# Kernel optimization log

Measured on AMD Instinct MI355X. Metric: run time of the kernel, lower is better.

Reference implementation:

```python
import jax, jax.numpy as jnp
import numpy as np

N = 50000        # num nodes
NFEAT = 512      # input feature dim
NCLASS = 256     # output classes (out_features of out_att)
E_RAND = 800000  # random edges; + N self-loops
NEG_SLOPE = 0.2  # leakyrelu alpha


def setup_inputs() -> dict:
    key = jax.random.key(0)
    k1, k2, k3, k4 = jax.random.split(key, 4)
    x = jax.random.normal(k1, (N, NFEAT), dtype=jnp.float32)
    W = jax.random.normal(k2, (NFEAT, NCLASS), dtype=jnp.float32) / np.float32(np.sqrt(NFEAT))
    a = jax.random.normal(k3, (2 * NCLASS,), dtype=jnp.float32) / np.float32(np.sqrt(2 * NCLASS))
    rand_edges = jax.random.randint(k4, (2, E_RAND), 0, N, dtype=jnp.int32)
    self_loops = jnp.tile(jnp.arange(N, dtype=jnp.int32), (2, 1))
    edge_index = jnp.concatenate([rand_edges, self_loops], axis=1)  # [2, E]
    return {"x": x, "W": W, "a": a, "edge_index": edge_index}


def reference(x, W, a, edge_index):
    # Eval-mode SpGAT: dropout is identity (training=False).
    row, col = edge_index[0], edge_index[1]  # edge = adj.nonzero().t(): row aggregates from col
    h = x @ W                                # [N, F]
    F_out = h.shape[1]
    # a @ cat(h[row], h[col]) == (h @ a1)[row] + (h @ a2)[col]  (avoids [E, 2F] concat)
    s_row = h @ a[:F_out]                    # [N]
    s_col = h @ a[F_out:]                    # [N]
    logits = s_row[row] + s_col[col]         # [E]
    e = jnp.exp(-jax.nn.leaky_relu(logits, negative_slope=NEG_SLOPE))  # [E]
    rowsum = jax.ops.segment_sum(e, row, num_segments=N)               # [N]
    msgs = e[:, None] * h[col]                                         # [E, F]
    h_prime = jax.ops.segment_sum(msgs, row, num_segments=N) / rowsum[:, None]
    return jax.nn.log_softmax(jax.nn.elu(h_prime), axis=1)
```

## Files before the change

### kernel.cpp

```cpp
#include <hip/hip_runtime.h>
#include <math.h>

#define NNODES   50000
#define NFEAT    512
#define NCLASS   256
#define NEG_SLOPE 0.2f
#define GBLK     782
#define SBLK     196
#define BCAP     64

typedef __attribute__((ext_vector_type(8))) short short8;
typedef __attribute__((ext_vector_type(4))) float floatx4;

__device__ __forceinline__ unsigned short f2bf(float f) {
    unsigned u = __builtin_bit_cast(unsigned, f);
    u += 0x7fffu + ((u >> 16) & 1u);
    return (unsigned short)(u >> 16);
}
__device__ __forceinline__ float bf2f_lo(unsigned u) {
    return __builtin_bit_cast(float, u << 16);
}
__device__ __forceinline__ float bf2f_hi(unsigned u) {
    return __builtin_bit_cast(float, u & 0xffff0000u);
}
__device__ __forceinline__ unsigned pack_bf16_rh(float lo, float hi) {
    const unsigned ulo = __builtin_bit_cast(unsigned, lo) + 0x8000u;
    const unsigned uhi = __builtin_bit_cast(unsigned, hi) + 0x8000u;
    return __builtin_amdgcn_perm(uhi, ulo, 0x07060302);
}

#if __has_builtin(__builtin_amdgcn_fdot2_f32_bf16)
#define HAVE_DOT2 1
typedef __attribute__((ext_vector_type(2))) __bf16 bfx2;
__device__ __forceinline__ float dot2bf(unsigned hpair, unsigned epair, float acc) {
    return __builtin_amdgcn_fdot2_f32_bf16(__builtin_bit_cast(bfx2, hpair),
                                           __builtin_bit_cast(bfx2, epair), acc, false);
}
#endif

__global__ __launch_bounds__(256) void init_kernel(const float* __restrict__ W,
                                                   unsigned short* __restrict__ Wt,
                                                   int* __restrict__ cursor, int zn) {
    const int i = blockIdx.x * 256 + threadIdx.x;
    const int n = i >> 9;
    const int k = i & 511;
    Wt[i] = f2bf(W[(size_t)k * NCLASS + n]);
    if (i < zn) cursor[i] = 0;
}

__global__ __launch_bounds__(256, 4) void gemm_scatter_kernel(const float* __restrict__ x,
                                                              const unsigned short* __restrict__ Wt,
                                                              unsigned short* __restrict__ hb,
                                                              const float* __restrict__ a,
                                                              float* __restrict__ s_row,
                                                              float* __restrict__ s_col,
                                                              const int* __restrict__ erow,
                                                              const int* __restrict__ ecol,
                                                              int* __restrict__ cursor,
                                                              int* __restrict__ bucket,
                                                              int M, int E) {
    __shared__ union {
        struct { short As[2][64 * 32]; short Bs[2][256 * 32]; } k;
        short Cs[32 * 260];
    } u;

    const int bid = blockIdx.x;
    const int tid = threadIdx.x;

    if (bid < SBLK) {
        const int stride = SBLK * 256;
        for (int i = bid * 256 + tid; i < E; i += stride) {
            const int r = erow[i];
            const int c = ecol[i];
            const int pos = atomicAdd(&cursor[r], 1);
            if (pos < BCAP) bucket[((size_t)r << 6) + pos] = c;
        }
        return;
    }

    const int w    = tid >> 6;
    const int lane = tid & 63;
    const int rowbase = (bid - SBLK) * 64;

    const int wm = w & 1;
    const int wn = w >> 1;
    const int srow = lane >> 2;
    const int skq  = (lane & 3) << 3;
    const int fm = lane & 15;
    const int fq = lane >> 4;

    floatx4 acc[2][8];
#pragma unroll
    for (int i = 0; i < 2; ++i)
#pragma unroll
        for (int j = 0; j < 8; ++j)
            acc[i][j] = (floatx4){0.f, 0.f, 0.f, 0.f};

    const int arow = min(rowbase + w * 16 + srow, M - 1);
    const size_t abase = (size_t)arow * NFEAT + skq;
    const int lrowA = (w * 16 + srow) * 32 + skq;

#define STAGE_B(buf, k0)                                                                      \
    {                                                                                         \
        _Pragma("unroll")                                                                     \
        for (int t = 0; t < 4; ++t) {                                                         \
            const int seg = w * 4 + t;                                                        \
            const int nr  = seg * 16 + srow;                                                  \
            __builtin_amdgcn_global_load_lds(                                                 \
                (const __attribute__((address_space(1))) void*)(Wt + (size_t)nr * NFEAT + (k0) + skq), \
                (__attribute__((address_space(3))) void*)(&u.k.Bs[buf][seg * 512]), 16, 0, 0); \
        }                                                                                     \
    }

    STAGE_B(0, 0)
    {
        const float4* xp = (const float4*)&x[abase];
        const float4 u0 = xp[0];
        const float4 u1 = xp[1];
        uint4 o;
        o.x = pack_bf16_rh(u0.x, u0.y);
        o.y = pack_bf16_rh(u0.z, u0.w);
        o.z = pack_bf16_rh(u1.x, u1.y);
        o.w = pack_bf16_rh(u1.z, u1.w);
        *(uint4*)&u.k.As[0][lrowA] = o;
    }
    __syncthreads();

    int cur = 0;
    for (int k0 = 0; k0 < NFEAT; k0 += 32) {
        const int nxt = cur ^ 1;
        const bool have_next = (k0 + 32) < NFEAT;
        float4 p0, p1;
        if (have_next) {
            const float4* xp = (const float4*)&x[abase + k0 + 32];
            p0 = xp[0];
            p1 = xp[1];
            STAGE_B(nxt, k0 + 32)
        }

        short8 af[2];
#pragma unroll
        for (int mt = 0; mt < 2; ++mt)
            af[mt] = *(const short8*)&u.k.As[cur][(wm * 32 + mt * 16 + fm) * 32 + fq * 8];
#pragma unroll
        for (int nt = 0; nt < 8; ++nt) {
            const short8 bfr = *(const short8*)&u.k.Bs[cur][(wn * 128 + nt * 16 + fm) * 32 + fq * 8];
            acc[0][nt] = __builtin_amdgcn_mfma_f32_16x16x32_bf16(af[0], bfr, acc[0][nt], 0, 0, 0);
            acc[1][nt] = __builtin_amdgcn_mfma_f32_16x16x32_bf16(af[1], bfr, acc[1][nt], 0, 0, 0);
        }

        if (have_next) {
            uint4 o;
            o.x = pack_bf16_rh(p0.x, p0.y);
            o.y = pack_bf16_rh(p0.z, p0.w);
            o.z = pack_bf16_rh(p1.x, p1.y);
            o.w = pack_bf16_rh(p1.z, p1.w);
            *(uint4*)&u.k.As[nxt][lrowA] = o;
        }
        __syncthreads();
        cur = nxt;
    }

#pragma unroll
    for (int p = 0; p < 2; ++p) {
        __syncthreads();
        if (wm == p) {
#pragma unroll
            for (int mt = 0; mt < 2; ++mt)
#pragma unroll
                for (int nt = 0; nt < 8; ++nt)
#pragma unroll
                    for (int r = 0; r < 4; ++r)
                        u.Cs[(mt * 16 + fq * 4 + r) * 260 + wn * 128 + nt * 16 + fm] =
                            (short)f2bf(acc[mt][nt][r]);
        }
        __syncthreads();
#pragma unroll
        for (int kk = 0; kk < 8; ++kk) {
            const int idx = tid + kk * 256;
            const int lrow = idx >> 6;
            const int c4 = (idx & 63) << 2;
            const int grow = rowbase + p * 32 + lrow;
            const uint2 vv = *(const uint2*)&u.Cs[lrow * 260 + c4];
            const float f0 = bf2f_lo(vv.x), f1 = bf2f_hi(vv.x);
            const float f2 = bf2f_lo(vv.y), f3 = bf2f_hi(vv.y);
            const float4 A1 = *(const float4*)&a[c4];
            const float4 A2 = *(const float4*)&a[NCLASS + c4];
            float p1 = f0 * A1.x + f1 * A1.y + f2 * A1.z + f3 * A1.w;
            float p2 = f0 * A2.x + f1 * A2.y + f2 * A2.z + f3 * A2.w;
#pragma unroll
            for (int off = 1; off < 64; off <<= 1) {
                p1 += __shfl_xor(p1, off);
                p2 += __shfl_xor(p2, off);
            }
            if (grow < M) {
                *(uint2*)&hb[(size_t)grow * NCLASS + c4] = vv;
                if (lane == 0) {
                    s_row[grow] = p1;
                    s_col[grow] = p2;
                }
            }
        }
    }
}

__global__ __launch_bounds__(256) void aggregate_kernel(const unsigned short* __restrict__ hb,
                                                        const int* __restrict__ bucket,
                                                        const int* __restrict__ cnt,
                                                        const float* __restrict__ s_row,
                                                        const float* __restrict__ s_col,
                                                        float* __restrict__ out, int n) {
    const int wave = (int)((blockIdx.x * (size_t)blockDim.x + threadIdx.x) >> 6);
    const int lane = threadIdx.x & 63;
    if (wave >= n) return;
    const int r = wave;
    const int jb = r << 6;
    const int je = jb + min(cnt[r], BCAP);
    const int fo = lane << 2;
    const float sr = s_row[r];

    float rowsum = 0.f;
    int j = jb;

#define EDGE_E(c) ({ const float _l = sr + s_col[c];                         \
                     const float _lr = _l > 0.f ? _l : NEG_SLOPE * _l;       \
                     __expf(-_lr); })

#ifdef HAVE_DOT2
    float ac0 = 0.f, ac1 = 0.f, ac2 = 0.f, ac3 = 0.f;
    for (; j + 3 < je; j += 4) {
        const int4 cv = *(const int4*)&bucket[j];
        const uint2 g0 = *(const uint2*)&hb[(size_t)cv.x * NCLASS + fo];
        const uint2 g1 = *(const uint2*)&hb[(size_t)cv.y * NCLASS + fo];
        const uint2 g2 = *(const uint2*)&hb[(size_t)cv.z * NCLASS + fo];
        const uint2 g3 = *(const uint2*)&hb[(size_t)cv.w * NCLASS + fo];
        const float e0 = EDGE_E(cv.x);
        const float e1 = EDGE_E(cv.y);
        const float e2 = EDGE_E(cv.z);
        const float e3 = EDGE_E(cv.w);
        const unsigned ep01 = pack_bf16_rh(e0, e1);
        const unsigned ep23 = pack_bf16_rh(e2, e3);
        rowsum += (e0 + e1) + (e2 + e3);
        ac0 = dot2bf(__builtin_amdgcn_perm(g1.x, g0.x, 0x05040100), ep01, ac0);
        ac1 = dot2bf(__builtin_amdgcn_perm(g1.x, g0.x, 0x07060302), ep01, ac1);
        ac2 = dot2bf(__builtin_amdgcn_perm(g1.y, g0.y, 0x05040100), ep01, ac2);
        ac3 = dot2bf(__builtin_amdgcn_perm(g1.y, g0.y, 0x07060302), ep01, ac3);
        ac0 = dot2bf(__builtin_amdgcn_perm(g3.x, g2.x, 0x05040100), ep23, ac0);
        ac1 = dot2bf(__builtin_amdgcn_perm(g3.x, g2.x, 0x07060302), ep23, ac1);
        ac2 = dot2bf(__builtin_amdgcn_perm(g3.y, g2.y, 0x05040100), ep23, ac2);
        ac3 = dot2bf(__builtin_amdgcn_perm(g3.y, g2.y, 0x07060302), ep23, ac3);
    }
    float4 acc = make_float4(ac0, ac1, ac2, ac3);
#else
    float4 acc = make_float4(0.f, 0.f, 0.f, 0.f);
    for (; j + 3 < je; j += 4) {
        const int4 cv = *(const int4*)&bucket[j];
        const uint2 g0 = *(const uint2*)&hb[(size_t)cv.x * NCLASS + fo];
        const uint2 g1 = *(const uint2*)&hb[(size_t)cv.y * NCLASS + fo];
        const uint2 g2 = *(const uint2*)&hb[(size_t)cv.z * NCLASS + fo];
        const uint2 g3 = *(const uint2*)&hb[(size_t)cv.w * NCLASS + fo];
        const float e0 = EDGE_E(cv.x);
        const float e1 = EDGE_E(cv.y);
        const float e2 = EDGE_E(cv.z);
        const float e3 = EDGE_E(cv.w);
        rowsum += (e0 + e1) + (e2 + e3);
        acc.x += e0 * bf2f_lo(g0.x) + e1 * bf2f_lo(g1.x) + e2 * bf2f_lo(g2.x) + e3 * bf2f_lo(g3.x);
        acc.y += e0 * bf2f_hi(g0.x) + e1 * bf2f_hi(g1.x) + e2 * bf2f_hi(g2.x) + e3 * bf2f_hi(g3.x);
        acc.z += e0 * bf2f_lo(g0.y) + e1 * bf2f_lo(g1.y) + e2 * bf2f_lo(g2.y) + e3 * bf2f_lo(g3.y);
        acc.w += e0 * bf2f_hi(g0.y) + e1 * bf2f_hi(g1.y) + e2 * bf2f_hi(g2.y) + e3 * bf2f_hi(g3.y);
    }
#endif
    for (; j < je; ++j) {
        const int c = bucket[j];
        const uint2 g = *(const uint2*)&hb[(size_t)c * NCLASS + fo];
        const float e = EDGE_E(c);
        rowsum += e;
        acc.x += e * bf2f_lo(g.x);
        acc.y += e * bf2f_hi(g.x);
        acc.z += e * bf2f_lo(g.y);
        acc.w += e * bf2f_hi(g.y);
    }

    const float inv = 1.f / rowsum;
    float v[4] = {acc.x * inv, acc.y * inv, acc.z * inv, acc.w * inv};
#pragma unroll
    for (int i = 0; i < 4; ++i)
        v[i] = v[i] > 0.f ? v[i] : __expf(v[i]) - 1.f;

    float m = fmaxf(fmaxf(v[0], v[1]), fmaxf(v[2], v[3]));
#pragma unroll
    for (int off = 32; off > 0; off >>= 1) m = fmaxf(m, __shfl_xor(m, off));
    float s = 0.f;
#pragma unroll
    for (int i = 0; i < 4; ++i) s += __expf(v[i] - m);
#pragma unroll
    for (int off = 32; off > 0; off >>= 1) s += __shfl_xor(s, off);
    const float lse = m + __logf(s);

    float4 o = make_float4(v[0] - lse, v[1] - lse, v[2] - lse, v[3] - lse);
    *(float4*)&out[(size_t)r * NCLASS + fo] = o;
}

extern "C" void kernel_launch(void* const* d_in, const int* in_sizes, int n_in,
                              void* d_out, int out_size, void* d_ws, size_t ws_size,
                              hipStream_t stream) {
    const float* x  = (const float*)d_in[0];
    const float* W  = (const float*)d_in[1];
    const float* a  = (const float*)d_in[2];
    const int* edge = (const int*)d_in[3];
    float* out = (float*)d_out;

    const int M = in_sizes[0] / NFEAT;
    const int E = in_sizes[3] / 2;
    const int* row = edge;
    const int* col = edge + E;

    char* ws = (char*)d_ws;
    size_t off = 0;
    auto carve = [&](size_t bytes) -> char* {
        char* p = ws + off;
        off = (off + bytes + 255) & ~(size_t)255;
        return p;
    };
    unsigned short* Wt = (unsigned short*)carve((size_t)NCLASS * NFEAT * sizeof(short));
    unsigned short* hb = (unsigned short*)carve((size_t)M * NCLASS * sizeof(short));
    int*   cursor   = (int*)carve((size_t)M * sizeof(int));
    float* s_row    = (float*)carve((size_t)M * sizeof(float));
    float* s_col    = (float*)carve((size_t)M * sizeof(float));
    int*   bucket   = (int*)carve((size_t)M * BCAP * sizeof(int));

    init_kernel<<<512, 256, 0, stream>>>(W, Wt, cursor, M);

    gemm_scatter_kernel<<<SBLK + GBLK, 256, 0, stream>>>(x, Wt, hb, a, s_row, s_col,
                                                         row, col, cursor, bucket, M, E);

    aggregate_kernel<<<(M + 3) / 4, 256, 0, stream>>>(hb, bucket, cursor, s_row, s_col, out, M);
}
```

Before: 282.5 us.

## Enlarge GEMM row tile to 128 and rebalance scatter block count

Doubles the GEMM block M-tile from 64 to 128 rows, so each wave computes 64x128 with 4x8 MFMA accumulators and reuses each B fragment across four A fragments. The goal is to halve the redundant Wt staging traffic per output row and raise MFMA density. It also raises the edge-scatter block count to match the GEMM block count, which changes how the fused kernel splits its work. The cost is more registers and shared memory per block, which lowers the occupancy hint from 4 to 3 blocks per CU. The epilogue now runs four 32-row passes through the Cs buffer.

Result: slower. 364.5 us (+29.0%).

```diff
diff --git a/kernel.cpp b/kernel.cpp
--- a/kernel.cpp
+++ b/kernel.cpp
@@ -5,8 +5,8 @@
 #define NFEAT    512
 #define NCLASS   256
 #define NEG_SLOPE 0.2f
-#define GBLK     782
-#define SBLK     196
+#define GBLK     391
+#define SBLK     391
 #define BCAP     64
 
 typedef __attribute__((ext_vector_type(8))) short short8;
@@ -48,7 +48,7 @@
     if (i < zn) cursor[i] = 0;
 }
 
-__global__ __launch_bounds__(256, 4) void gemm_scatter_kernel(const float* __restrict__ x,
+__global__ __launch_bounds__(256, 3) void gemm_scatter_kernel(const float* __restrict__ x,
                                                               const unsigned short* __restrict__ Wt,
                                                               unsigned short* __restrict__ hb,
                                                               const float* __restrict__ a,
@@ -60,7 +60,7 @@
                                                               int* __restrict__ bucket,
                                                               int M, int E) {
     __shared__ union {
-        struct { short As[2][64 * 32]; short Bs[2][256 * 32]; } k;
+        struct { short As[2][128 * 32]; short Bs[2][256 * 32]; } k;
         short Cs[32 * 260];
     } u;
 
@@ -80,7 +80,7 @@
 
     const int w    = tid >> 6;
     const int lane = tid & 63;
-    const int rowbase = (bid - SBLK) * 64;
+    const int rowbase = (bid - SBLK) * 128;
 
     const int wm = w & 1;
     const int wn = w >> 1;
@@ -89,16 +89,19 @@
     const int fm = lane & 15;
     const int fq = lane >> 4;
 
-    floatx4 acc[2][8];
-#pragma unroll
-    for (int i = 0; i < 2; ++i)
+    floatx4 acc[4][8];
+#pragma unroll
+    for (int i = 0; i < 4; ++i)
 #pragma unroll
         for (int j = 0; j < 8; ++j)
             acc[i][j] = (floatx4){0.f, 0.f, 0.f, 0.f};
 
-    const int arow = min(rowbase + w * 16 + srow, M - 1);
-    const size_t abase = (size_t)arow * NFEAT + skq;
-    const int lrowA = (w * 16 + srow) * 32 + skq;
+    const int ar0 = min(rowbase + w * 32 + srow, M - 1);
+    const int ar1 = min(rowbase + w * 32 + 16 + srow, M - 1);
+    const size_t ab0 = (size_t)ar0 * NFEAT + skq;
+    const size_t ab1 = (size_t)ar1 * NFEAT + skq;
+    const int lr0 = (w * 32 + srow) * 32 + skq;
+    const int lr1 = (w * 32 + 16 + srow) * 32 + skq;
 
 #define STAGE_B(buf, k0)                                                                      \
     {                                                                                         \
@@ -112,41 +115,48 @@
         }                                                                                     \
     }
 
+#define PACK_A(dst_off, srcp)                                                                 \
+    {                                                                                         \
+        const float4 u0 = (srcp)[0];                                                          \
+        const float4 u1 = (srcp)[1];                                                          \
+        uint4 o;                                                                              \
+        o.x = pack_bf16_rh(u0.x, u0.y);                                                       \
+        o.y = pack_bf16_rh(u0.z, u0.w);                                                       \
+        o.z = pack_bf16_rh(u1.x, u1.y);                                                       \
+        o.w = pack_bf16_rh(u1.z, u1.w);                                                       \
+        *(uint4*)&u.k.As[0][dst_off] = o;                                                     \
+    }
+
     STAGE_B(0, 0)
-    {
-        const float4* xp = (const float4*)&x[abase];
-        const float4 u0 = xp[0];
-        const float4 u1 = xp[1];
-        uint4 o;
-        o.x = pack_bf16_rh(u0.x, u0.y);
-        o.y = pack_bf16_rh(u0.z, u0.w);
-        o.z = pack_bf16_rh(u1.x, u1.y);
-        o.w = pack_bf16_rh(u1.z, u1.w);
-        *(uint4*)&u.k.As[0][lrowA] = o;
-    }
+    PACK_A(lr0, (const float4*)&x[ab0])
+    PACK_A(lr1, (const float4*)&x[ab1])
     __syncthreads();
 
     int cur = 0;
     for (int k0 = 0; k0 < NFEAT; k0 += 32) {
         const int nxt = cur ^ 1;
         const bool have_next = (k0 + 32) < NFEAT;
-        float4 p0, p1;
+        float4 p0, p1, q0, q1;
         if (have_next) {
-            const float4* xp = (const float4*)&x[abase + k0 + 32];
-            p0 = xp[0];
-            p1 = xp[1];
+            const float4* xp0 = (const float4*)&x[ab0 + k0 + 32];
+            const float4* xp1 = (const float4*)&x[ab1 + k0 + 32];
+            p0 = xp0[0];
+            p1 = xp0[1];
+            q0 = xp1[0];
+            q1 = xp1[1];
             STAGE_B(nxt, k0 + 32)
         }
 
-        short8 af[2];
-#pragma unroll
-        for (int mt = 0; mt < 2; ++mt)
-            af[mt] = *(const short8*)&u.k.As[cur][(wm * 32 + mt * 16 + fm) * 32 + fq * 8];
+        short8 af[4];
+#pragma unroll
+        for (int mt = 0; mt < 4; ++mt)
+            af[mt] = *(const short8*)&u.k.As[cur][(wm * 64 + mt * 16 + fm) * 32 + fq * 8];
 #pragma unroll
         for (int nt = 0; nt < 8; ++nt) {
             const short8 bfr = *(const short8*)&u.k.Bs[cur][(wn * 128 + nt * 16 + fm) * 32 + fq * 8];
-            acc[0][nt] = __builtin_amdgcn_mfma_f32_16x16x32_bf16(af[0], bfr, acc[0][nt], 0, 0, 0);
-            acc[1][nt] = __builtin_amdgcn_mfma_f32_16x16x32_bf16(af[1], bfr, acc[1][nt], 0, 0, 0);
+#pragma unroll
+            for (int mt = 0; mt < 4; ++mt)
+                acc[mt][nt] = __builtin_amdgcn_mfma_f32_16x16x32_bf16(af[mt], bfr, acc[mt][nt], 0, 0, 0);
         }
 
         if (have_next) {
@@ -155,24 +165,32 @@
             o.y = pack_bf16_rh(p0.z, p0.w);
             o.z = pack_bf16_rh(p1.x, p1.y);
             o.w = pack_bf16_rh(p1.z, p1.w);
-            *(uint4*)&u.k.As[nxt][lrowA] = o;
+            *(uint4*)&u.k.As[nxt][lr0] = o;
+            uint4 o2;
+            o2.x = pack_bf16_rh(q0.x, q0.y);
+            o2.y = pack_bf16_rh(q0.z, q0.w);
+            o2.z = pack_bf16_rh(q1.x, q1.y);
+            o2.w = pack_bf16_rh(q1.z, q1.w);
+            *(uint4*)&u.k.As[nxt][lr1] = o2;
         }
         __syncthreads();
         cur = nxt;
     }
 
 #pragma unroll
-    for (int p = 0; p < 2; ++p) {
+    for (int p = 0; p < 4; ++p) {
         __syncthreads();
-        if (wm == p) {
-#pragma unroll
-            for (int mt = 0; mt < 2; ++mt)
+        if ((w & 1) == (p >> 1)) {
+#pragma unroll
+            for (int mt2 = 0; mt2 < 2; ++mt2) {
+                const int mt = (p & 1) * 2 + mt2;
 #pragma unroll
                 for (int nt = 0; nt < 8; ++nt)
 #pragma unroll
                     for (int r = 0; r < 4; ++r)
-                        u.Cs[(mt * 16 + fq * 4 + r) * 260 + wn * 128 + nt * 16 + fm] =
+                        u.Cs[(mt2 * 16 + fq * 4 + r) * 260 + wn * 128 + nt * 16 + fm] =
                             (short)f2bf(acc[mt][nt][r]);
+            }
         }
         __syncthreads();
 #pragma unroll
```
